# Kernel tuning notes

Hardware: AMD Instinct MI355X
Metric: run time of the kernel (lower is better)

Reference implementation:

```python
import jax, jax.numpy as jnp
import numpy as np
from jax import lax

B, S, T = 64, 256, 16
V, E = 262, 64
H = E // 2  # GRU hidden per direction


def setup_inputs() -> dict:
    key = jax.random.key(0)
    ks = jax.random.split(key, 10)
    x = jax.random.randint(ks[0], (B, S, T), 0, V, dtype=jnp.int64).astype(jnp.int32)
    scale = 1.0 / np.sqrt(H)
    emb = jax.random.normal(ks[1], (V, E), dtype=jnp.float32) * 0.1
    emb = emb.at[0].set(0.0)  # padding_idx=0
    def u(k, shape):
        return jax.random.uniform(k, shape, jnp.float32, -scale, scale)
    return {
        'x': x,
        'emb': emb,
        'Wih_f': u(ks[2], (3 * H, E)), 'Whh_f': u(ks[3], (3 * H, H)),
        'bih_f': u(ks[4], (3 * H,)),   'bhh_f': u(ks[5], (3 * H,)),
        'Wih_b': u(ks[6], (3 * H, E)), 'Whh_b': u(ks[7], (3 * H, H)),
        'bih_b': u(ks[8], (3 * H,)),   'bhh_b': u(ks[9], (3 * H,)),
    }


def _gru_dir(xe, Wih, Whh, bih, bhh, reverse):
    # xe: [N, T, E] -> outputs [N, T, H]; PyTorch GRU cell math.
    N = xe.shape[0]
    gi_all = jnp.einsum('nte,ge->ntg', xe, Wih) + bih  # precompute input gates [N,T,3H]

    def step(h, gi):
        gh = h @ Whh.T + bhh
        i_r, i_z, i_n = jnp.split(gi, 3, axis=-1)
        h_r, h_z, h_n = jnp.split(gh, 3, axis=-1)
        r = jax.nn.sigmoid(i_r + h_r)
        z = jax.nn.sigmoid(i_z + h_z)
        n = jnp.tanh(i_n + r * h_n)
        h_new = (1.0 - z) * n + z * h
        return h_new, h_new

    h0 = jnp.zeros((N, H), dtype=xe.dtype)
    _, ys = lax.scan(step, h0, jnp.swapaxes(gi_all, 0, 1), reverse=reverse)  # [T,N,H]
    return jnp.swapaxes(ys, 0, 1)


def reference(x, emb, Wih_f, Whh_f, bih_f, bhh_f, Wih_b, Whh_b, bih_b, bhh_b):
    xe = emb[x].reshape(B * S, T, E)  # embedding lookup, flatten words
    y_f = _gru_dir(xe, Wih_f, Whh_f, bih_f, bhh_f, reverse=False)
    y_b = _gru_dir(xe, Wih_b, Whh_b, bih_b, bhh_b, reverse=True)
    y = jnp.concatenate([y_f, y_b], axis=-1)  # [B*S, T, 2H]
    out = jnp.max(y, axis=1)  # temporal max-pool over chars
    return out.reshape(B, S, 2 * H)
```

## Files before the change

kernel.cpp:

```cpp
#include <hip/hip_runtime.h>
#include <math.h>

#define NW 16384
#define Tt 16
#define Vv 262
#define Ee 64
#define Hh 32
#define G3 96

#define GFLOATS  (2*Vv*G3)
#define BHI_FOFF GFLOATS
#define BLO_FOFF (GFLOATS + 3072)

typedef float        f32x4  __attribute__((ext_vector_type(4)));
typedef short        bf16x8 __attribute__((ext_vector_type(8)));
typedef unsigned int u32;
typedef u32          u32x4  __attribute__((ext_vector_type(4)));
typedef int          i32x4  __attribute__((ext_vector_type(4)));

__device__ __forceinline__ unsigned short bf16_rtne(float f) {
    u32 u = __builtin_bit_cast(u32, f);
    u += 0x7fffu + ((u >> 16) & 1u);
    return (unsigned short)(u >> 16);
}

__device__ __forceinline__ u32 pk_bf16(float lo, float hi) {
    u32 r;
    asm("v_cvt_pk_bf16_f32 %0, %1, %2" : "=v"(r) : "v"(lo), "v"(hi));
    return r;
}

__device__ __forceinline__ float fsigm(float x) {
    return __builtin_amdgcn_rcpf(1.0f + __expf(-x));
}
__device__ __forceinline__ float ftanh(float x) {
    return 1.0f - 2.0f * __builtin_amdgcn_rcpf(1.0f + __expf(2.0f * x));
}

__global__ __launch_bounds__(256) void precomp(
    const float* __restrict__ emb,
    const float* __restrict__ Wih_f, const float* __restrict__ Whh_f,
    const float* __restrict__ bih_f, const float* __restrict__ bhh_f,
    const float* __restrict__ Wih_b, const float* __restrict__ Whh_b,
    const float* __restrict__ bih_b, const float* __restrict__ bhh_b,
    float* __restrict__ ws)
{
    int b = blockIdx.x;
    if (b < 197) {
        int idx = b * 256 + threadIdx.x;
        if (idx >= GFLOATS) return;
        int dir = idx / (Vv * G3);
        int rem = idx - dir * (Vv * G3);
        int v = rem / G3;
        int g = rem - v * G3;
        const float* Wih = dir ? Wih_b : Wih_f;
        float acc = (dir ? bih_b : bih_f)[g];
        if (g < 64) acc += (dir ? bhh_b : bhh_f)[g];
        const f32x4* er = (const f32x4*)(emb + v * Ee);
        const f32x4* wr = (const f32x4*)(Wih + g * Ee);
        float s = 0.0f;
        #pragma unroll
        for (int e = 0; e < 16; ++e) {
            f32x4 a = er[e], w = wr[e];
            s = fmaf(a[0], w[0], s);
            s = fmaf(a[1], w[1], s);
            s = fmaf(a[2], w[2], s);
            s = fmaf(a[3], w[3], s);
        }
        ws[idx] = acc + s;
    } else {
        int t = (b - 197) * 256 + threadIdx.x;
        if (t >= 768) return;
        int dir = t / 384;
        int r2  = t - dir * 384;
        int c   = r2 >> 6;
        int l   = r2 & 63;
        int m   = l & 15, q = l >> 4;
        const float* Whh = dir ? Whh_b : Whh_f;
        const float* row = Whh + (16 * c + m) * Hh + 8 * q;
        u32 hiw[4], low[4];
        #pragma unroll
        for (int p = 0; p < 4; ++p) {
            float f0 = row[2 * p], f1 = row[2 * p + 1];
            unsigned short h0 = bf16_rtne(f0), h1 = bf16_rtne(f1);
            float rr0 = f0 - __builtin_bit_cast(float, (u32)h0 << 16);
            float rr1 = f1 - __builtin_bit_cast(float, (u32)h1 << 16);
            unsigned short l0 = bf16_rtne(rr0), l1 = bf16_rtne(rr1);
            hiw[p] = (u32)h0 | ((u32)h1 << 16);
            low[p] = (u32)l0 | ((u32)l1 << 16);
        }
        u32x4* dh = (u32x4*)(ws + BHI_FOFF) + (dir * 6 + c) * 64 + l;
        u32x4* dl = (u32x4*)(ws + BLO_FOFF) + (dir * 6 + c) * 64 + l;
        u32x4 vh = {hiw[0], hiw[1], hiw[2], hiw[3]};
        u32x4 vl = {low[0], low[1], low[2], low[3]};
        *dh = vh;
        *dl = vl;
    }
}

__global__ __launch_bounds__(256, 2) void gru_main(
    const int*   __restrict__ x,
    const float* __restrict__ ws,
    const float* __restrict__ bhh_f,
    const float* __restrict__ bhh_b,
    float*       __restrict__ out)
{
    __shared__ float hbuf[4][16 * 33];
    __shared__ int   chs[4][16 * 17];

    const int tid  = threadIdx.x;
    const int lane = tid & 63;
    const int widx = tid >> 6;
    const int wave = blockIdx.x * 4 + widx;
    const int dir  = wave & 1;
    const int wg   = wave >> 1;
    const int m = lane & 15, q = lane >> 4;

    {
        i32x4 cv = *(const i32x4*)(x + wg * 256 + lane * 4);
        #pragma unroll
        for (int j = 0; j < 4; ++j) {
            int p = lane * 4 + j;
            chs[widx][(p >> 4) * 17 + (p & 15)] = cv[j];
        }
    }

    bf16x8 bhi[6], blo[6];
    {
        const u32x4* ph = (const u32x4*)(ws + BHI_FOFF) + dir * 384 + lane;
        const u32x4* pl = (const u32x4*)(ws + BLO_FOFF) + dir * 384 + lane;
        #pragma unroll
        for (int c = 0; c < 6; ++c) {
            bhi[c] = __builtin_bit_cast(bf16x8, ph[c * 64]);
            blo[c] = __builtin_bit_cast(bf16x8, pl[c * 64]);
        }
    }
    const float* bhh = dir ? bhh_b : bhh_f;
    const float bn0 = bhh[64 + m];
    const float bn1 = bhh[80 + m];
    const float* Gt = ws + dir * (Vv * G3);

    f32x4 h0v = {0.f, 0.f, 0.f, 0.f};
    f32x4 h1v = {0.f, 0.f, 0.f, 0.f};
    f32x4 mx0 = {-3e38f, -3e38f, -3e38f, -3e38f};
    f32x4 mx1 = {-3e38f, -3e38f, -3e38f, -3e38f};

    float* hb = hbuf[widx];
    int*   ch = chs[widx];
    const int t0 = dir ? 15 : 0;
    const int sg = dir ? -1 : 1;

    int cw0 = ch[(4 * q + 0) * 17 + t0];
    int cw1 = ch[(4 * q + 1) * 17 + t0];
    int cw2 = ch[(4 * q + 2) * 17 + t0];
    int cw3 = ch[(4 * q + 3) * 17 + t0];

    #pragma unroll 1
    for (int t = 0; t < 16; ++t) {
        float gr0[4], gr1[4], gz0[4], gz1[4], gn0[4], gn1[4];
        {
            int cwr[4] = {cw0, cw1, cw2, cw3};
            #pragma unroll
            for (int r = 0; r < 4; ++r) {
                const float* gp = Gt + cwr[r] * G3 + m;
                gr0[r] = gp[0];  gr1[r] = gp[16];
                gz0[r] = gp[32]; gz1[r] = gp[48];
                gn0[r] = gp[64]; gn1[r] = gp[80];
            }
        }
        int nw0 = cw0, nw1 = cw1, nw2 = cw2, nw3 = cw3;
        if (t < 15) {
            int tt = t0 + sg * (t + 1);
            nw0 = ch[(4 * q + 0) * 17 + tt];
            nw1 = ch[(4 * q + 1) * 17 + tt];
            nw2 = ch[(4 * q + 2) * 17 + tt];
            nw3 = ch[(4 * q + 3) * 17 + tt];
        }
        #pragma unroll
        for (int r = 0; r < 4; ++r) {
            hb[(4 * q + r) * 33 + m]      = h0v[r];
            hb[(4 * q + r) * 33 + 16 + m] = h1v[r];
        }
        float a0 = hb[m * 33 + 8 * q + 0];
        float a1 = hb[m * 33 + 8 * q + 1];
        float a2 = hb[m * 33 + 8 * q + 2];
        float a3 = hb[m * 33 + 8 * q + 3];
        float a4 = hb[m * 33 + 8 * q + 4];
        float a5 = hb[m * 33 + 8 * q + 5];
        float a6 = hb[m * 33 + 8 * q + 6];
        float a7 = hb[m * 33 + 8 * q + 7];
        u32 w0 = pk_bf16(a0, a1), w1 = pk_bf16(a2, a3);
        u32 w2 = pk_bf16(a4, a5), w3 = pk_bf16(a6, a7);
        float e0 = __builtin_bit_cast(float, w0 << 16);
        float o0 = __builtin_bit_cast(float, w0 & 0xffff0000u);
        float e1 = __builtin_bit_cast(float, w1 << 16);
        float o1 = __builtin_bit_cast(float, w1 & 0xffff0000u);
        float e2 = __builtin_bit_cast(float, w2 << 16);
        float o2 = __builtin_bit_cast(float, w2 & 0xffff0000u);
        float e3 = __builtin_bit_cast(float, w3 << 16);
        float o3 = __builtin_bit_cast(float, w3 & 0xffff0000u);
        u32 v0 = pk_bf16(a0 - e0, a1 - o0);
        u32 v1 = pk_bf16(a2 - e1, a3 - o1);
        u32 v2 = pk_bf16(a4 - e2, a5 - o2);
        u32 v3 = pk_bf16(a6 - e3, a7 - o3);
        u32x4 hiq = {w0, w1, w2, w3};
        u32x4 loq = {v0, v1, v2, v3};
        bf16x8 Ahi = __builtin_bit_cast(bf16x8, hiq);
        bf16x8 Alo = __builtin_bit_cast(bf16x8, loq);

        f32x4 ar0 = {gr0[0], gr0[1], gr0[2], gr0[3]};
        f32x4 ar1 = {gr1[0], gr1[1], gr1[2], gr1[3]};
        f32x4 az0 = {gz0[0], gz0[1], gz0[2], gz0[3]};
        f32x4 az1 = {gz1[0], gz1[1], gz1[2], gz1[3]};
        f32x4 an0 = {bn0, bn0, bn0, bn0};
        f32x4 an1 = {bn1, bn1, bn1, bn1};
        ar0 = __builtin_amdgcn_mfma_f32_16x16x32_bf16(Alo, bhi[0], ar0, 0, 0, 0);
        ar0 = __builtin_amdgcn_mfma_f32_16x16x32_bf16(Ahi, blo[0], ar0, 0, 0, 0);
        ar0 = __builtin_amdgcn_mfma_f32_16x16x32_bf16(Ahi, bhi[0], ar0, 0, 0, 0);
        ar1 = __builtin_amdgcn_mfma_f32_16x16x32_bf16(Alo, bhi[1], ar1, 0, 0, 0);
        ar1 = __builtin_amdgcn_mfma_f32_16x16x32_bf16(Ahi, blo[1], ar1, 0, 0, 0);
        ar1 = __builtin_amdgcn_mfma_f32_16x16x32_bf16(Ahi, bhi[1], ar1, 0, 0, 0);
        az0 = __builtin_amdgcn_mfma_f32_16x16x32_bf16(Alo, bhi[2], az0, 0, 0, 0);
        az0 = __builtin_amdgcn_mfma_f32_16x16x32_bf16(Ahi, blo[2], az0, 0, 0, 0);
        az0 = __builtin_amdgcn_mfma_f32_16x16x32_bf16(Ahi, bhi[2], az0, 0, 0, 0);
        az1 = __builtin_amdgcn_mfma_f32_16x16x32_bf16(Alo, bhi[3], az1, 0, 0, 0);
        az1 = __builtin_amdgcn_mfma_f32_16x16x32_bf16(Ahi, blo[3], az1, 0, 0, 0);
        az1 = __builtin_amdgcn_mfma_f32_16x16x32_bf16(Ahi, bhi[3], az1, 0, 0, 0);
        an0 = __builtin_amdgcn_mfma_f32_16x16x32_bf16(Alo, bhi[4], an0, 0, 0, 0);
        an0 = __builtin_amdgcn_mfma_f32_16x16x32_bf16(Ahi, blo[4], an0, 0, 0, 0);
        an0 = __builtin_amdgcn_mfma_f32_16x16x32_bf16(Ahi, bhi[4], an0, 0, 0, 0);
        an1 = __builtin_amdgcn_mfma_f32_16x16x32_bf16(Alo, bhi[5], an1, 0, 0, 0);
        an1 = __builtin_amdgcn_mfma_f32_16x16x32_bf16(Ahi, blo[5], an1, 0, 0, 0);
        an1 = __builtin_amdgcn_mfma_f32_16x16x32_bf16(Ahi, bhi[5], an1, 0, 0, 0);

        #pragma unroll
        for (int r = 0; r < 4; ++r) {
            float rr0 = fsigm(ar0[r]);
            float zz0 = fsigm(az0[r]);
            float nn0 = ftanh(fmaf(rr0, an0[r], gn0[r]));
            float hx0 = nn0 + zz0 * (h0v[r] - nn0);
            mx0[r] = fmaxf(mx0[r], hx0);
            h0v[r] = hx0;

            float rr1 = fsigm(ar1[r]);
            float zz1 = fsigm(az1[r]);
            float nn1 = ftanh(fmaf(rr1, an1[r], gn1[r]));
            float hx1 = nn1 + zz1 * (h1v[r] - nn1);
            mx1[r] = fmaxf(mx1[r], hx1);
            h1v[r] = hx1;
        }
        cw0 = nw0; cw1 = nw1; cw2 = nw2; cw3 = nw3;
    }

    const int ob = wg * 16 * 64 + dir * 32;
    #pragma unroll
    for (int r = 0; r < 4; ++r) {
        out[ob + (4 * q + r) * 64 + m]      = mx0[r];
        out[ob + (4 * q + r) * 64 + 16 + m] = mx1[r];
    }
}

extern "C" void kernel_launch(void* const* d_in, const int* in_sizes, int n_in,
                              void* d_out, int out_size, void* d_ws, size_t ws_size,
                              hipStream_t stream) {
    const int*   x     = (const int*)  d_in[0];
    const float* emb   = (const float*)d_in[1];
    const float* Wih_f = (const float*)d_in[2];
    const float* Whh_f = (const float*)d_in[3];
    const float* bih_f = (const float*)d_in[4];
    const float* bhh_f = (const float*)d_in[5];
    const float* Wih_b = (const float*)d_in[6];
    const float* Whh_b = (const float*)d_in[7];
    const float* bih_b = (const float*)d_in[8];
    const float* bhh_b = (const float*)d_in[9];
    float* out = (float*)d_out;
    float* ws  = (float*)d_ws;

    precomp<<<200, 256, 0, stream>>>(emb, Wih_f, Whh_f, bih_f, bhh_f,
                                     Wih_b, Whh_b, bih_b, bhh_b, ws);
    gru_main<<<512, 256, 0, stream>>>(x, ws, bhh_f, bhh_b, out);
}
```

Measured before the change: 96.44 us.

## Interleave gate table per row, double-buffer gate loads, peel first GRU step

```diff
diff --git a/kernel.cpp b/kernel.cpp
--- a/kernel.cpp
+++ b/kernel.cpp
@@ -4,11 +4,12 @@
 #define NW 16384
 #define Tt 16
 #define Vv 262
-#define Ee 64
 #define Hh 32
-#define G3 96
-
-#define GFLOATS  (2*Vv*G3)
+
+#define GROWF 8
+#define GPERV (16*GROWF)
+#define GDIR  (Vv*GPERV)
+#define GFLOATS (2*GDIR)
 #define BHI_FOFF GFLOATS
 #define BLO_FOFF (GFLOATS + 3072)
 
@@ -23,13 +24,11 @@
     u += 0x7fffu + ((u >> 16) & 1u);
     return (unsigned short)(u >> 16);
 }
-
-__device__ __forceinline__ u32 pk_bf16(float lo, float hi) {
+__device__ __forceinline__ u32 pk_bf16(float a, float b) {
     u32 r;
-    asm("v_cvt_pk_bf16_f32 %0, %1, %2" : "=v"(r) : "v"(lo), "v"(hi));
+    asm("v_cvt_pk_bf16_f32 %0, %1, %2" : "=v"(r) : "v"(a), "v"(b));
     return r;
 }
-
 __device__ __forceinline__ float fsigm(float x) {
     return __builtin_amdgcn_rcpf(1.0f + __expf(-x));
 }
@@ -46,30 +45,36 @@
     float* __restrict__ ws)
 {
     int b = blockIdx.x;
-    if (b < 197) {
+    if (b < 262) {
         int idx = b * 256 + threadIdx.x;
-        if (idx >= GFLOATS) return;
-        int dir = idx / (Vv * G3);
-        int rem = idx - dir * (Vv * G3);
-        int v = rem / G3;
-        int g = rem - v * G3;
-        const float* Wih = dir ? Wih_b : Wih_f;
-        float acc = (dir ? bih_b : bih_f)[g];
-        if (g < 64) acc += (dir ? bhh_b : bhh_f)[g];
-        const f32x4* er = (const f32x4*)(emb + v * Ee);
-        const f32x4* wr = (const f32x4*)(Wih + g * Ee);
-        float s = 0.0f;
-        #pragma unroll
-        for (int e = 0; e < 16; ++e) {
-            f32x4 a = er[e], w = wr[e];
-            s = fmaf(a[0], w[0], s);
-            s = fmaf(a[1], w[1], s);
-            s = fmaf(a[2], w[2], s);
-            s = fmaf(a[3], w[3], s);
-        }
-        ws[idx] = acc + s;
+        int dir = idx / GDIR;
+        int rem = idx - dir * GDIR;
+        int v   = rem / GPERV;
+        int r2  = rem - v * GPERV;
+        int m   = r2 >> 3;
+        int slot= r2 & 7;
+        float val = 0.0f;
+        if (slot < 6) {
+            int g = m + (slot & 1) * 16 + (slot >> 1) * 32;
+            const float* Wih = dir ? Wih_b : Wih_f;
+            float acc = (dir ? bih_b : bih_f)[g];
+            if (slot < 4) acc += (dir ? bhh_b : bhh_f)[g];
+            const f32x4* er = (const f32x4*)(emb + v * 64);
+            const f32x4* wr = (const f32x4*)(Wih + g * 64);
+            float s = 0.0f;
+            #pragma unroll
+            for (int e = 0; e < 16; ++e) {
+                f32x4 a = er[e], w = wr[e];
+                s = fmaf(a[0], w[0], s);
+                s = fmaf(a[1], w[1], s);
+                s = fmaf(a[2], w[2], s);
+                s = fmaf(a[3], w[3], s);
+            }
+            val = acc + s;
+        }
+        ws[idx] = val;
     } else {
-        int t = (b - 197) * 256 + threadIdx.x;
+        int t = (b - 262) * 256 + threadIdx.x;
         if (t >= 768) return;
         int dir = t / 384;
         int r2  = t - dir * 384;
@@ -105,7 +110,7 @@
     const float* __restrict__ bhh_b,
     float*       __restrict__ out)
 {
-    __shared__ float hbuf[4][16 * 33];
+    __shared__ float hbuf[4][16 * 36];
     __shared__ int   chs[4][16 * 17];
 
     const int tid  = threadIdx.x;
@@ -119,9 +124,9 @@
     {
         i32x4 cv = *(const i32x4*)(x + wg * 256 + lane * 4);
         #pragma unroll
-        for (int j = 0; j < 4; ++j) {
-            int p = lane * 4 + j;
-            chs[widx][(p >> 4) * 17 + (p & 15)] = cv[j];
+        for (int j2 = 0; j2 < 4; ++j2) {
+            int p = lane * 4 + j2;
+            chs[widx][(p >> 4) * 17 + (p & 15)] = cv[j2];
         }
     }
 
@@ -138,7 +143,9 @@
     const float* bhh = dir ? bhh_b : bhh_f;
     const float bn0 = bhh[64 + m];
     const float bn1 = bhh[80 + m];
-    const float* Gt = ws + dir * (Vv * G3);
+    const f32x4 an0c = {bn0, bn0, bn0, bn0};
+    const f32x4 an1c = {bn1, bn1, bn1, bn1};
+    const float* Gt = ws + dir * GDIR;
 
     f32x4 h0v = {0.f, 0.f, 0.f, 0.f};
     f32x4 h1v = {0.f, 0.f, 0.f, 0.f};
@@ -150,47 +157,59 @@
     const int t0 = dir ? 15 : 0;
     const int sg = dir ? -1 : 1;
 
-    int cw0 = ch[(4 * q + 0) * 17 + t0];
-    int cw1 = ch[(4 * q + 1) * 17 + t0];
-    int cw2 = ch[(4 * q + 2) * 17 + t0];
-    int cw3 = ch[(4 * q + 3) * 17 + t0];
-
-    #pragma unroll 1
-    for (int t = 0; t < 16; ++t) {
-        float gr0[4], gr1[4], gz0[4], gz1[4], gn0[4], gn1[4];
-        {
-            int cwr[4] = {cw0, cw1, cw2, cw3};
+    int ca[4];
+    f32x4 GA[8], GB[8];
+
+    auto gload = [&](f32x4 (&Gv)[8]) {
+        #pragma unroll
+        for (int r = 0; r < 4; ++r) {
+            const f32x4* gp = (const f32x4*)(Gt + ca[r] * GPERV + m * GROWF);
+            Gv[2 * r]     = gp[0];
+            Gv[2 * r + 1] = gp[1];
+        }
+    };
+    auto gates = [&](const f32x4& ar0, const f32x4& ar1,
+                     const f32x4& az0, const f32x4& az1,
+                     const f32x4& an0, const f32x4& an1,
+                     const f32x4 (&Gc)[8]) {
+        #pragma unroll
+        for (int r = 0; r < 4; ++r) {
+            float gn0 = Gc[2 * r + 1][0];
+            float gn1 = Gc[2 * r + 1][1];
+            float rr0 = fsigm(ar0[r]);
+            float zz0 = fsigm(az0[r]);
+            float nn0 = ftanh(fmaf(rr0, an0[r], gn0));
+            float hx0 = nn0 + zz0 * (h0v[r] - nn0);
+            mx0[r] = fmaxf(mx0[r], hx0);
+            h0v[r] = hx0;
+            hb[(4 * q + r) * 36 + m] = hx0;
+
+            float rr1 = fsigm(ar1[r]);
+            float zz1 = fsigm(az1[r]);
+            float nn1 = ftanh(fmaf(rr1, an1[r], gn1));
+            float hx1 = nn1 + zz1 * (h1v[r] - nn1);
+            mx1[r] = fmaxf(mx1[r], hx1);
+            h1v[r] = hx1;
+            hb[(4 * q + r) * 36 + 16 + m] = hx1;
+        }
+    };
+
+#define TRIPLE(acc, c) \
+    acc = __builtin_amdgcn_mfma_f32_16x16x32_bf16(Alo, bhi[c], acc, 0, 0, 0); \
+    acc = __builtin_amdgcn_mfma_f32_16x16x32_bf16(Ahi, blo[c], acc, 0, 0, 0); \
+    acc = __builtin_amdgcn_mfma_f32_16x16x32_bf16(Ahi, bhi[c], acc, 0, 0, 0);
+
+    auto step = [&](const f32x4 (&Gc)[8], f32x4 (&Gn)[8], int t) {
+        if (t < 15) gload(Gn);
+        if (t < 14) {
+            int s2 = t0 + (t + 2) * sg;
             #pragma unroll
-            for (int r = 0; r < 4; ++r) {
-                const float* gp = Gt + cwr[r] * G3 + m;
-                gr0[r] = gp[0];  gr1[r] = gp[16];
-                gz0[r] = gp[32]; gz1[r] = gp[48];
-                gn0[r] = gp[64]; gn1[r] = gp[80];
-            }
-        }
-        int nw0 = cw0, nw1 = cw1, nw2 = cw2, nw3 = cw3;
-        if (t < 15) {
-            int tt = t0 + sg * (t + 1);
-            nw0 = ch[(4 * q + 0) * 17 + tt];
-            nw1 = ch[(4 * q + 1) * 17 + tt];
-            nw2 = ch[(4 * q + 2) * 17 + tt];
-            nw3 = ch[(4 * q + 3) * 17 + tt];
-        }
-        #pragma unroll
-        for (int r = 0; r < 4; ++r) {
-            hb[(4 * q + r) * 33 + m]      = h0v[r];
-            hb[(4 * q + r) * 33 + 16 + m] = h1v[r];
-        }
-        float a0 = hb[m * 33 + 8 * q + 0];
-        float a1 = hb[m * 33 + 8 * q + 1];
-        float a2 = hb[m * 33 + 8 * q + 2];
-        float a3 = hb[m * 33 + 8 * q + 3];
-        float a4 = hb[m * 33 + 8 * q + 4];
-        float a5 = hb[m * 33 + 8 * q + 5];
-        float a6 = hb[m * 33 + 8 * q + 6];
-        float a7 = hb[m * 33 + 8 * q + 7];
-        u32 w0 = pk_bf16(a0, a1), w1 = pk_bf16(a2, a3);
-        u32 w2 = pk_bf16(a4, a5), w3 = pk_bf16(a6, a7);
+            for (int r = 0; r < 4; ++r) ca[r] = ch[(4 * q + r) * 17 + s2];
+        }
+        const f32x4 A0 = *(const f32x4*)(hb + m * 36 + 8 * q);
+        const f32x4 A1 = *(const f32x4*)(hb + m * 36 + 8 * q + 4);
+        u32 w0 = pk_bf16(A0[0], A0[1]), w1 = pk_bf16(A0[2], A0[3]);
+        u32 w2 = pk_bf16(A1[0], A1[1]), w3 = pk_bf16(A1[2], A1[3]);
         float e0 = __builtin_bit_cast(float, w0 << 16);
         float o0 = __builtin_bit_cast(float, w0 & 0xffff0000u);
         float e1 = __builtin_bit_cast(float, w1 << 16);
@@ -199,58 +218,53 @@
         float o2 = __builtin_bit_cast(float, w2 & 0xffff0000u);
         float e3 = __builtin_bit_cast(float, w3 << 16);
         float o3 = __builtin_bit_cast(float, w3 & 0xffff0000u);
-        u32 v0 = pk_bf16(a0 - e0, a1 - o0);
-        u32 v1 = pk_bf16(a2 - e1, a3 - o1);
-        u32 v2 = pk_bf16(a4 - e2, a5 - o2);
-        u32 v3 = pk_bf16(a6 - e3, a7 - o3);
+        u32 v0 = pk_bf16(A0[0] - e0, A0[1] - o0);
+        u32 v1 = pk_bf16(A0[2] - e1, A0[3] - o1);
+        u32 v2 = pk_bf16(A1[0] - e2, A1[1] - o2);
+        u32 v3 = pk_bf16(A1[2] - e3, A1[3] - o3);
         u32x4 hiq = {w0, w1, w2, w3};
         u32x4 loq = {v0, v1, v2, v3};
         bf16x8 Ahi = __builtin_bit_cast(bf16x8, hiq);
         bf16x8 Alo = __builtin_bit_cast(bf16x8, loq);
 
-        f32x4 ar0 = {gr0[0], gr0[1], gr0[2], gr0[3]};
-        f32x4 ar1 = {gr1[0], gr1[1], gr1[2], gr1[3]};
-        f32x4 az0 = {gz0[0], gz0[1], gz0[2], gz0[3]};
-        f32x4 az1 = {gz1[0], gz1[1], gz1[2], gz1[3]};
-        f32x4 an0 = {bn0, bn0, bn0, bn0};
-        f32x4 an1 = {bn1, bn1, bn1, bn1};
-        ar0 = __builtin_amdgcn_mfma_f32_16x16x32_bf16(Alo, bhi[0], ar0, 0, 0, 0);
-        ar0 = __builtin_amdgcn_mfma_f32_16x16x32_bf16(Ahi, blo[0], ar0, 0, 0, 0);
-        ar0 = __builtin_amdgcn_mfma_f32_16x16x32_bf16(Ahi, bhi[0], ar0, 0, 0, 0);
-        ar1 = __builtin_amdgcn_mfma_f32_16x16x32_bf16(Alo, bhi[1], ar1, 0, 0, 0);
-        ar1 = __builtin_amdgcn_mfma_f32_16x16x32_bf16(Ahi, blo[1], ar1, 0, 0, 0);
-        ar1 = __builtin_amdgcn_mfma_f32_16x16x32_bf16(Ahi, bhi[1], ar1, 0, 0, 0);
-        az0 = __builtin_amdgcn_mfma_f32_16x16x32_bf16(Alo, bhi[2], az0, 0, 0, 0);
-        az0 = __builtin_amdgcn_mfma_f32_16x16x32_bf16(Ahi, blo[2], az0, 0, 0, 0);
-        az0 = __builtin_amdgcn_mfma_f32_16x16x32_bf16(Ahi, bhi[2], az0, 0, 0, 0);
-        az1 = __builtin_amdgcn_mfma_f32_16x16x32_bf16(Alo, bhi[3], az1, 0, 0, 0);
-        az1 = __builtin_amdgcn_mfma_f32_16x16x32_bf16(Ahi, blo[3], az1, 0, 0, 0);
-        az1 = __builtin_amdgcn_mfma_f32_16x16x32_bf16(Ahi, bhi[3], az1, 0, 0, 0);
-        an0 = __builtin_amdgcn_mfma_f32_16x16x32_bf16(Alo, bhi[4], an0, 0, 0, 0);
-        an0 = __builtin_amdgcn_mfma_f32_16x16x32_bf16(Ahi, blo[4], an0, 0, 0, 0);
-        an0 = __builtin_amdgcn_mfma_f32_16x16x32_bf16(Ahi, bhi[4], an0, 0, 0, 0);
-        an1 = __builtin_amdgcn_mfma_f32_16x16x32_bf16(Alo, bhi[5], an1, 0, 0, 0);
-        an1 = __builtin_amdgcn_mfma_f32_16x16x32_bf16(Ahi, blo[5], an1, 0, 0, 0);
-        an1 = __builtin_amdgcn_mfma_f32_16x16x32_bf16(Ahi, bhi[5], an1, 0, 0, 0);
-
-        #pragma unroll
-        for (int r = 0; r < 4; ++r) {
-            float rr0 = fsigm(ar0[r]);
-            float zz0 = fsigm(az0[r]);
-            float nn0 = ftanh(fmaf(rr0, an0[r], gn0[r]));
-            float hx0 = nn0 + zz0 * (h0v[r] - nn0);
-            mx0[r] = fmaxf(mx0[r], hx0);
-            h0v[r] = hx0;
-
-            float rr1 = fsigm(ar1[r]);
-            float zz1 = fsigm(az1[r]);
-            float nn1 = ftanh(fmaf(rr1, an1[r], gn1[r]));
-            float hx1 = nn1 + zz1 * (h1v[r] - nn1);
-            mx1[r] = fmaxf(mx1[r], hx1);
-            h1v[r] = hx1;
-        }
-        cw0 = nw0; cw1 = nw1; cw2 = nw2; cw3 = nw3;
-    }
+        f32x4 ar0 = {Gc[0][0], Gc[2][0], Gc[4][0], Gc[6][0]};
+        f32x4 ar1 = {Gc[0][1], Gc[2][1], Gc[4][1], Gc[6][1]};
+        f32x4 az0 = {Gc[0][2], Gc[2][2], Gc[4][2], Gc[6][2]};
+        f32x4 az1 = {Gc[0][3], Gc[2][3], Gc[4][3], Gc[6][3]};
+        f32x4 an0 = an0c, an1 = an1c;
+        TRIPLE(ar0, 0)
+        TRIPLE(ar1, 1)
+        TRIPLE(az0, 2)
+        TRIPLE(az1, 3)
+        TRIPLE(an0, 4)
+        TRIPLE(an1, 5)
+        gates(ar0, ar1, az0, az1, an0, an1, Gc);
+    };
+
+    #pragma unroll
+    for (int r = 0; r < 4; ++r) ca[r] = ch[(4 * q + r) * 17 + t0];
+    gload(GA);
+    #pragma unroll
+    for (int r = 0; r < 4; ++r) ca[r] = ch[(4 * q + r) * 17 + t0 + sg];
+
+    gload(GB);
+    #pragma unroll
+    for (int r = 0; r < 4; ++r) ca[r] = ch[(4 * q + r) * 17 + t0 + 2 * sg];
+    {
+        f32x4 ar0 = {GA[0][0], GA[2][0], GA[4][0], GA[6][0]};
+        f32x4 ar1 = {GA[0][1], GA[2][1], GA[4][1], GA[6][1]};
+        f32x4 az0 = {GA[0][2], GA[2][2], GA[4][2], GA[6][2]};
+        f32x4 az1 = {GA[0][3], GA[2][3], GA[4][3], GA[6][3]};
+        gates(ar0, ar1, az0, az1, an0c, an1c, GA);
+    }
+
+    step(GB, GA, 1);
+    #pragma unroll 1
+    for (int it = 0; it < 7; ++it) {
+        step(GA, GB, 2 + 2 * it);
+        step(GB, GA, 3 + 2 * it);
+    }
+#undef TRIPLE
 
     const int ob = wg * 16 * 64 + dir * 32;
     #pragma unroll
@@ -276,7 +290,7 @@
     float* out = (float*)d_out;
     float* ws  = (float*)d_ws;
 
-    precomp<<<200, 256, 0, stream>>>(emb, Wih_f, Whh_f, bih_f, bhh_f,
+    precomp<<<265, 256, 0, stream>>>(emb, Wih_f, Whh_f, bih_f, bhh_f,
                                      Wih_b, Whh_b, bih_b, bhh_b, ws);
     gru_main<<<512, 256, 0, stream>>>(x, ws, bhh_f, bhh_b, out);
 }
```

Measured after the change: 98.80 us. +2.4%, slower.

## Transpose GRU MFMA so hidden stays in registers, double-buffer gate loads

Applied to the files above, without the earlier changes.

```diff
diff --git a/kernel.cpp b/kernel.cpp
--- a/kernel.cpp
+++ b/kernel.cpp
@@ -4,11 +4,11 @@
 #define NW 16384
 #define Tt 16
 #define Vv 262
-#define Ee 64
 #define Hh 32
 #define G3 96
 
-#define GFLOATS  (2*Vv*G3)
+#define GDIRF    (Vv*G3)
+#define GFLOATS  (2*GDIRF)
 #define BHI_FOFF GFLOATS
 #define BLO_FOFF (GFLOATS + 3072)
 
@@ -23,13 +23,11 @@
     u += 0x7fffu + ((u >> 16) & 1u);
     return (unsigned short)(u >> 16);
 }
-
-__device__ __forceinline__ u32 pk_bf16(float lo, float hi) {
+__device__ __forceinline__ u32 pk_bf16(float a, float b) {
     u32 r;
-    asm("v_cvt_pk_bf16_f32 %0, %1, %2" : "=v"(r) : "v"(lo), "v"(hi));
+    asm("v_cvt_pk_bf16_f32 %0, %1, %2" : "=v"(r) : "v"(a), "v"(b));
     return r;
 }
-
 __device__ __forceinline__ float fsigm(float x) {
     return __builtin_amdgcn_rcpf(1.0f + __expf(-x));
 }
@@ -49,15 +47,15 @@
     if (b < 197) {
         int idx = b * 256 + threadIdx.x;
         if (idx >= GFLOATS) return;
-        int dir = idx / (Vv * G3);
-        int rem = idx - dir * (Vv * G3);
+        int dir = idx / GDIRF;
+        int rem = idx - dir * GDIRF;
         int v = rem / G3;
         int g = rem - v * G3;
         const float* Wih = dir ? Wih_b : Wih_f;
         float acc = (dir ? bih_b : bih_f)[g];
         if (g < 64) acc += (dir ? bhh_b : bhh_f)[g];
-        const f32x4* er = (const f32x4*)(emb + v * Ee);
-        const f32x4* wr = (const f32x4*)(Wih + g * Ee);
+        const f32x4* er = (const f32x4*)(emb + v * 64);
+        const f32x4* wr = (const f32x4*)(Wih + g * 64);
         float s = 0.0f;
         #pragma unroll
         for (int e = 0; e < 16; ++e) {
@@ -105,8 +103,7 @@
     const float* __restrict__ bhh_b,
     float*       __restrict__ out)
 {
-    __shared__ float hbuf[4][16 * 33];
-    __shared__ int   chs[4][16 * 17];
+    __shared__ int chs[4][16 * 17];
 
     const int tid  = threadIdx.x;
     const int lane = tid & 63;
@@ -119,145 +116,130 @@
     {
         i32x4 cv = *(const i32x4*)(x + wg * 256 + lane * 4);
         #pragma unroll
-        for (int j = 0; j < 4; ++j) {
-            int p = lane * 4 + j;
-            chs[widx][(p >> 4) * 17 + (p & 15)] = cv[j];
-        }
-    }
-
-    bf16x8 bhi[6], blo[6];
+        for (int j2 = 0; j2 < 4; ++j2) {
+            int p = lane * 4 + j2;
+            chs[widx][(p >> 4) * 17 + (p & 15)] = cv[j2];
+        }
+    }
+
+    bf16x8 whi[6], wlo[6];
     {
         const u32x4* ph = (const u32x4*)(ws + BHI_FOFF) + dir * 384 + lane;
         const u32x4* pl = (const u32x4*)(ws + BLO_FOFF) + dir * 384 + lane;
         #pragma unroll
         for (int c = 0; c < 6; ++c) {
-            bhi[c] = __builtin_bit_cast(bf16x8, ph[c * 64]);
-            blo[c] = __builtin_bit_cast(bf16x8, pl[c * 64]);
+            whi[c] = __builtin_bit_cast(bf16x8, ph[c * 64]);
+            wlo[c] = __builtin_bit_cast(bf16x8, pl[c * 64]);
         }
     }
     const float* bhh = dir ? bhh_b : bhh_f;
-    const float bn0 = bhh[64 + m];
-    const float bn1 = bhh[80 + m];
-    const float* Gt = ws + dir * (Vv * G3);
-
-    f32x4 h0v = {0.f, 0.f, 0.f, 0.f};
-    f32x4 h1v = {0.f, 0.f, 0.f, 0.f};
-    f32x4 mx0 = {-3e38f, -3e38f, -3e38f, -3e38f};
-    f32x4 mx1 = {-3e38f, -3e38f, -3e38f, -3e38f};
-
-    float* hb = hbuf[widx];
-    int*   ch = chs[widx];
+    const f32x4 bnA = *(const f32x4*)(bhh + 64 + 4 * q);
+    const f32x4 bnB = *(const f32x4*)(bhh + 80 + 4 * q);
+    const float* Gt = ws + dir * GDIRF;
+
+    f32x4 hA = {0.f, 0.f, 0.f, 0.f};
+    f32x4 hB = {0.f, 0.f, 0.f, 0.f};
+    f32x4 mxA = {-3e38f, -3e38f, -3e38f, -3e38f};
+    f32x4 mxB = {-3e38f, -3e38f, -3e38f, -3e38f};
+
+    int* ch = chs[widx];
     const int t0 = dir ? 15 : 0;
     const int sg = dir ? -1 : 1;
 
-    int cw0 = ch[(4 * q + 0) * 17 + t0];
-    int cw1 = ch[(4 * q + 1) * 17 + t0];
-    int cw2 = ch[(4 * q + 2) * 17 + t0];
-    int cw3 = ch[(4 * q + 3) * 17 + t0];
-
+    f32x4 GA[6], GB[6];
+    int cn;
+
+    auto gload = [&](f32x4 (&G)[6], int v) {
+        const float* gp = Gt + v * G3 + 4 * q;
+        #pragma unroll
+        for (int c = 0; c < 6; ++c) G[c] = *(const f32x4*)(gp + 16 * c);
+    };
+
+    auto gates = [&](const f32x4 (&acc)[6], const f32x4& gnA, const f32x4& gnB) {
+        #pragma unroll
+        for (int r = 0; r < 4; ++r) {
+            float rr = fsigm(acc[0][r]);
+            float zz = fsigm(acc[2][r]);
+            float nn = ftanh(fmaf(rr, acc[4][r], gnA[r]));
+            float hx = nn + zz * (hA[r] - nn);
+            mxA[r] = fmaxf(mxA[r], hx);
+            hA[r] = hx;
+
+            float rb = fsigm(acc[1][r]);
+            float zb = fsigm(acc[3][r]);
+            float nb = ftanh(fmaf(rb, acc[5][r], gnB[r]));
+            float hy = nb + zb * (hB[r] - nb);
+            mxB[r] = fmaxf(mxB[r], hy);
+            hB[r] = hy;
+        }
+    };
+
+    auto bfly = [&](u32& k0, u32& k1, u32& k2, u32& k3) {
+        asm volatile("v_permlane32_swap_b32 %0, %1" : "+v"(k0), "+v"(k2));
+        asm volatile("v_permlane32_swap_b32 %0, %1" : "+v"(k1), "+v"(k3));
+        asm volatile("v_permlane16_swap_b32 %0, %1" : "+v"(k0), "+v"(k2));
+        asm volatile("v_permlane16_swap_b32 %0, %1" : "+v"(k1), "+v"(k3));
+    };
+
+    auto mkfrag = [&](bf16x8& Bhi, bf16x8& Blo) {
+        u32 k0 = pk_bf16(hA[0], hA[1]), k1 = pk_bf16(hA[2], hA[3]);
+        u32 k2 = pk_bf16(hB[0], hB[1]), k3 = pk_bf16(hB[2], hB[3]);
+        float e0 = __builtin_bit_cast(float, k0 << 16);
+        float o0 = __builtin_bit_cast(float, k0 & 0xffff0000u);
+        float e1 = __builtin_bit_cast(float, k1 << 16);
+        float o1 = __builtin_bit_cast(float, k1 & 0xffff0000u);
+        float e2 = __builtin_bit_cast(float, k2 << 16);
+        float o2 = __builtin_bit_cast(float, k2 & 0xffff0000u);
+        float e3 = __builtin_bit_cast(float, k3 << 16);
+        float o3 = __builtin_bit_cast(float, k3 & 0xffff0000u);
+        u32 l0 = pk_bf16(hA[0] - e0, hA[1] - o0);
+        u32 l1 = pk_bf16(hA[2] - e1, hA[3] - o1);
+        u32 l2 = pk_bf16(hB[0] - e2, hB[1] - o2);
+        u32 l3 = pk_bf16(hB[2] - e3, hB[3] - o3);
+        bfly(k0, k1, k2, k3);
+        bfly(l0, l1, l2, l3);
+        u32x4 hq = {k0, k1, k2, k3};
+        u32x4 lq = {l0, l1, l2, l3};
+        Bhi = __builtin_bit_cast(bf16x8, hq);
+        Blo = __builtin_bit_cast(bf16x8, lq);
+    };
+
+    auto step = [&](const f32x4 (&Gc)[6], f32x4 (&Gn)[6], int t) {
+        if (t < 15) gload(Gn, cn);
+        if (t < 14) cn = ch[m * 17 + t0 + (t + 2) * sg];
+        bf16x8 Bhi, Blo;
+        mkfrag(Bhi, Blo);
+        f32x4 acc[6] = {Gc[0], Gc[1], Gc[2], Gc[3], bnA, bnB};
+        #pragma unroll
+        for (int c = 0; c < 6; ++c) {
+            acc[c] = __builtin_amdgcn_mfma_f32_16x16x32_bf16(wlo[c], Bhi, acc[c], 0, 0, 0);
+            acc[c] = __builtin_amdgcn_mfma_f32_16x16x32_bf16(whi[c], Blo, acc[c], 0, 0, 0);
+            acc[c] = __builtin_amdgcn_mfma_f32_16x16x32_bf16(whi[c], Bhi, acc[c], 0, 0, 0);
+        }
+        gates(acc, Gc[4], Gc[5]);
+    };
+
+    int c0 = ch[m * 17 + t0];
+    gload(GA, c0);
+    int c1 = ch[m * 17 + t0 + sg];
+    gload(GB, c1);
+    cn = ch[m * 17 + t0 + 2 * sg];
+
+    {
+        f32x4 acc[6] = {GA[0], GA[1], GA[2], GA[3], bnA, bnB};
+        gates(acc, GA[4], GA[5]);
+    }
+
+    step(GB, GA, 1);
     #pragma unroll 1
-    for (int t = 0; t < 16; ++t) {
-        float gr0[4], gr1[4], gz0[4], gz1[4], gn0[4], gn1[4];
-        {
-            int cwr[4] = {cw0, cw1, cw2, cw3};
-            #pragma unroll
-            for (int r = 0; r < 4; ++r) {
-                const float* gp = Gt + cwr[r] * G3 + m;
-                gr0[r] = gp[0];  gr1[r] = gp[16];
-                gz0[r] = gp[32]; gz1[r] = gp[48];
-                gn0[r] = gp[64]; gn1[r] = gp[80];
-            }
-        }
-        int nw0 = cw0, nw1 = cw1, nw2 = cw2, nw3 = cw3;
-        if (t < 15) {
-            int tt = t0 + sg * (t + 1);
-            nw0 = ch[(4 * q + 0) * 17 + tt];
-            nw1 = ch[(4 * q + 1) * 17 + tt];
-            nw2 = ch[(4 * q + 2) * 17 + tt];
-            nw3 = ch[(4 * q + 3) * 17 + tt];
-        }
-        #pragma unroll
-        for (int r = 0; r < 4; ++r) {
-            hb[(4 * q + r) * 33 + m]      = h0v[r];
-            hb[(4 * q + r) * 33 + 16 + m] = h1v[r];
-        }
-        float a0 = hb[m * 33 + 8 * q + 0];
-        float a1 = hb[m * 33 + 8 * q + 1];
-        float a2 = hb[m * 33 + 8 * q + 2];
-        float a3 = hb[m * 33 + 8 * q + 3];
-        float a4 = hb[m * 33 + 8 * q + 4];
-        float a5 = hb[m * 33 + 8 * q + 5];
-        float a6 = hb[m * 33 + 8 * q + 6];
-        float a7 = hb[m * 33 + 8 * q + 7];
-        u32 w0 = pk_bf16(a0, a1), w1 = pk_bf16(a2, a3);
-        u32 w2 = pk_bf16(a4, a5), w3 = pk_bf16(a6, a7);
-        float e0 = __builtin_bit_cast(float, w0 << 16);
-        float o0 = __builtin_bit_cast(float, w0 & 0xffff0000u);
-        float e1 = __builtin_bit_cast(float, w1 << 16);
-        float o1 = __builtin_bit_cast(float, w1 & 0xffff0000u);
-        float e2 = __builtin_bit_cast(float, w2 << 16);
-        float o2 = __builtin_bit_cast(float, w2 & 0xffff0000u);
-        float e3 = __builtin_bit_cast(float, w3 << 16);
-        float o3 = __builtin_bit_cast(float, w3 & 0xffff0000u);
-        u32 v0 = pk_bf16(a0 - e0, a1 - o0);
-        u32 v1 = pk_bf16(a2 - e1, a3 - o1);
-        u32 v2 = pk_bf16(a4 - e2, a5 - o2);
-        u32 v3 = pk_bf16(a6 - e3, a7 - o3);
-        u32x4 hiq = {w0, w1, w2, w3};
-        u32x4 loq = {v0, v1, v2, v3};
-        bf16x8 Ahi = __builtin_bit_cast(bf16x8, hiq);
-        bf16x8 Alo = __builtin_bit_cast(bf16x8, loq);
-
-        f32x4 ar0 = {gr0[0], gr0[1], gr0[2], gr0[3]};
-        f32x4 ar1 = {gr1[0], gr1[1], gr1[2], gr1[3]};
-        f32x4 az0 = {gz0[0], gz0[1], gz0[2], gz0[3]};
-        f32x4 az1 = {gz1[0], gz1[1], gz1[2], gz1[3]};
-        f32x4 an0 = {bn0, bn0, bn0, bn0};
-        f32x4 an1 = {bn1, bn1, bn1, bn1};
-        ar0 = __builtin_amdgcn_mfma_f32_16x16x32_bf16(Alo, bhi[0], ar0, 0, 0, 0);
-        ar0 = __builtin_amdgcn_mfma_f32_16x16x32_bf16(Ahi, blo[0], ar0, 0, 0, 0);
-        ar0 = __builtin_amdgcn_mfma_f32_16x16x32_bf16(Ahi, bhi[0], ar0, 0, 0, 0);
-        ar1 = __builtin_amdgcn_mfma_f32_16x16x32_bf16(Alo, bhi[1], ar1, 0, 0, 0);
-        ar1 = __builtin_amdgcn_mfma_f32_16x16x32_bf16(Ahi, blo[1], ar1, 0, 0, 0);
-        ar1 = __builtin_amdgcn_mfma_f32_16x16x32_bf16(Ahi, bhi[1], ar1, 0, 0, 0);
-        az0 = __builtin_amdgcn_mfma_f32_16x16x32_bf16(Alo, bhi[2], az0, 0, 0, 0);
-        az0 = __builtin_amdgcn_mfma_f32_16x16x32_bf16(Ahi, blo[2], az0, 0, 0, 0);
-        az0 = __builtin_amdgcn_mfma_f32_16x16x32_bf16(Ahi, bhi[2], az0, 0, 0, 0);
-        az1 = __builtin_amdgcn_mfma_f32_16x16x32_bf16(Alo, bhi[3], az1, 0, 0, 0);
-        az1 = __builtin_amdgcn_mfma_f32_16x16x32_bf16(Ahi, blo[3], az1, 0, 0, 0);
-        az1 = __builtin_amdgcn_mfma_f32_16x16x32_bf16(Ahi, bhi[3], az1, 0, 0, 0);
-        an0 = __builtin_amdgcn_mfma_f32_16x16x32_bf16(Alo, bhi[4], an0, 0, 0, 0);
-        an0 = __builtin_amdgcn_mfma_f32_16x16x32_bf16(Ahi, blo[4], an0, 0, 0, 0);
-        an0 = __builtin_amdgcn_mfma_f32_16x16x32_bf16(Ahi, bhi[4], an0, 0, 0, 0);
-        an1 = __builtin_amdgcn_mfma_f32_16x16x32_bf16(Alo, bhi[5], an1, 0, 0, 0);
-        an1 = __builtin_amdgcn_mfma_f32_16x16x32_bf16(Ahi, blo[5], an1, 0, 0, 0);
-        an1 = __builtin_amdgcn_mfma_f32_16x16x32_bf16(Ahi, bhi[5], an1, 0, 0, 0);
-
-        #pragma unroll
-        for (int r = 0; r < 4; ++r) {
-            float rr0 = fsigm(ar0[r]);
-            float zz0 = fsigm(az0[r]);
-            float nn0 = ftanh(fmaf(rr0, an0[r], gn0[r]));
-            float hx0 = nn0 + zz0 * (h0v[r] - nn0);
-            mx0[r] = fmaxf(mx0[r], hx0);
-            h0v[r] = hx0;
-
-            float rr1 = fsigm(ar1[r]);
-            float zz1 = fsigm(az1[r]);
-            float nn1 = ftanh(fmaf(rr1, an1[r], gn1[r]));
-            float hx1 = nn1 + zz1 * (h1v[r] - nn1);
-            mx1[r] = fmaxf(mx1[r], hx1);
-            h1v[r] = hx1;
-        }
-        cw0 = nw0; cw1 = nw1; cw2 = nw2; cw3 = nw3;
-    }
-
-    const int ob = wg * 16 * 64 + dir * 32;
-    #pragma unroll
-    for (int r = 0; r < 4; ++r) {
-        out[ob + (4 * q + r) * 64 + m]      = mx0[r];
-        out[ob + (4 * q + r) * 64 + 16 + m] = mx1[r];
-    }
+    for (int it = 0; it < 7; ++it) {
+        step(GA, GB, 2 + 2 * it);
+        step(GB, GA, 3 + 2 * it);
+    }
+
+    const int ob = (wg * 16 + m) * 64 + dir * 32 + 4 * q;
+    *(f32x4*)(out + ob)      = mxA;
+    *(f32x4*)(out + ob + 16) = mxB;
 }
 
 extern "C" void kernel_launch(void* const* d_in, const int* in_sizes, int n_in,
```

New measurement: 101.5 us. +5.2%, slower.
